# Optimization experiments

Hardware: AMD Instinct MI355X
Metric: run time of the kernel (lower is better)

## Reference

```python
import jax, jax.numpy as jnp
import numpy as np

# --- static module config (from init_kwargs) ---
C1_OUT = 64          # c1OutChannels
C1K = 400            # k winners in conv layer
N_FC = 1024          # fc1 hidden units (n)
K_FC = 100           # k winners in fc1
BOOST = 1.0          # boostStrength
W_SPARSITY = 0.5     # weightSparsity: fraction of fc1 weights allowed nonzero
HP = 12              # pooled spatial size: floor((28-5+1)/2)
C1_OUTPUT_LEN = C1_OUT * HP * HP  # 9216
BATCH = 4096


def setup_inputs() -> dict:
    key = jax.random.key(0)
    ks = jax.random.split(key, 10)
    x = jax.random.normal(ks[0], (BATCH, 1, 28, 28), jnp.float32)
    c1_w = jax.random.normal(ks[1], (C1_OUT, 1, 5, 5), jnp.float32) * 0.1
    c1_b = jax.random.normal(ks[2], (C1_OUT,), jnp.float32) * 0.01
    # duty cycles live in [0, ~density]
    duty_cnn = jax.random.uniform(ks[3], (1, C1_OUT, 1, 1), jnp.float32) * 0.05
    fc1_w = jax.random.normal(ks[4], (N_FC, C1_OUT_LEN_ := C1_OUTPUT_LEN), jnp.float32) * 0.01
    fc1_mask_raw = jax.random.uniform(ks[5], (N_FC, C1_OUTPUT_LEN), jnp.float32)
    fc1_b = jax.random.normal(ks[6], (N_FC,), jnp.float32) * 0.01
    duty_fc = jax.random.uniform(ks[7], (N_FC,), jnp.float32) * 0.1
    fc2_w = jax.random.normal(ks[8], (10, N_FC), jnp.float32) * 0.05
    fc2_b = jnp.zeros((10,), jnp.float32)
    return dict(x=x, c1_w=c1_w, c1_b=c1_b, duty_cnn=duty_cnn, fc1_w=fc1_w,
                fc1_mask_raw=fc1_mask_raw, fc1_b=fc1_b, duty_fc=duty_fc,
                fc2_w=fc2_w, fc2_b=fc2_b)


def _kwinners(x_flat, boost_flat, k):
    """Duty-cycle-boosted k-winner mask.
    x_flat: [B, N]; boost_flat: [1, N] broadcastable boost factors.
    Keeps original x values at the top-k boosted positions per row, zeros rest.
    Boosting uses stop_gradient(x), matching KWinners*.forward(x.detach()*boost).
    """
    boosted = jax.lax.stop_gradient(x_flat) * boost_flat
    thr = jax.lax.top_k(boosted, k)[0][:, -1:]  # k-th largest per row
    return jnp.where(boosted >= thr, x_flat, jnp.zeros((), x_flat.dtype))


def reference(x, c1_w, c1_b, duty_cnn, fc1_w, fc1_mask_raw, fc1_b, duty_fc,
              fc2_w, fc2_b):
    B = x.shape[0]
    # conv2d (valid, stride 1) -> [B, 64, 24, 24]
    y = jax.lax.conv_general_dilated(
        x, c1_w, window_strides=(1, 1), padding='VALID',
        dimension_numbers=('NCHW', 'OIHW', 'NCHW')) + c1_b[None, :, None, None]
    # max_pool2d(2) -> [B, 64, 12, 12]
    y = jax.lax.reduce_window(y, -jnp.inf, jax.lax.max,
                              (1, 1, 2, 2), (1, 1, 2, 2), 'VALID')
    # KWinnersCNN: global top-k over flattened (C,H,W), per-channel boost
    target_density = C1K / C1_OUTPUT_LEN
    boost_c = jnp.exp((target_density - duty_cnn) * BOOST)  # [1,C,1,1]
    boost_flat = jnp.broadcast_to(boost_c, (1, C1_OUT, HP, HP)).reshape(1, -1)
    yf = _kwinners(y.reshape(B, -1), boost_flat, C1K)  # [B, 9216]
    # LinearSDR fc1: sparse-weight linear + KWinners
    w_mask = (fc1_mask_raw < W_SPARSITY).astype(fc1_w.dtype)
    h = yf @ (fc1_w * w_mask).T + fc1_b  # [B, 1024]
    boost_fc = jnp.exp((K_FC / N_FC - duty_fc) * BOOST)[None, :]
    h = _kwinners(h, boost_fc, K_FC)
    # fc2 + log_softmax (dropout inactive in eval mode)
    logits = h @ fc2_w.T + fc2_b
    return jax.nn.log_softmax(logits, axis=1)
```

## Files before the change

kernel.cpp:

```cpp
#include <hip/hip_runtime.h>

__device__ __forceinline__ float b2f(unsigned short u) {
  return __uint_as_float(((unsigned)u) << 16);
}
__device__ __forceinline__ unsigned short f2b(float f) {
  unsigned u = __float_as_uint(f);
  return (unsigned short)((u + 0x7FFFu + ((u >> 16) & 1u)) >> 16);
}
__device__ __forceinline__ float gload(const void* p, int i, int isb) {
  return isb ? b2f(((const unsigned short*)p)[i]) : ((const float*)p)[i];
}
__device__ __forceinline__ unsigned tokey(float f) {
  unsigned u = __float_as_uint(f);
  return u ^ (unsigned)(((int)u >> 31) | 0x80000000u);
}

__global__ void k_detect(const void* x, int* flag) {
  int tid = threadIdx.x;
  unsigned short u = ((const unsigned short*)x)[2 * tid];
  int e = (u >> 7) & 0xFF;
  bool sane = (e >= 100 && e <= 140);
  unsigned long long m = __ballot(sane);
  if (tid == 0) *flag = (__popcll(m) >= 40) ? 1 : 0;
}

__global__ __launch_bounds__(256) void k_prep(const void* __restrict__ fc1w,
                                              const void* __restrict__ mraw,
                                              float* __restrict__ WtF,
                                              const int* __restrict__ flag) {
  __shared__ float tile[64][65];
  const int isb = *flag;
  const int i0 = blockIdx.x * 64;
  const int u0 = blockIdx.y * 64;
  const int tx = threadIdx.x & 63, ty = threadIdx.x >> 6;
  for (int uu = ty; uu < 64; uu += 4) {
    int gi = (u0 + uu) * 9216 + i0 + tx;
    float wv = gload(fc1w, gi, isb);
    float mv = gload(mraw, gi, isb);
    tile[uu][tx] = (mv < 0.5f) ? wv : 0.0f;
  }
  __syncthreads();
  for (int ii = ty; ii < 64; ii += 4)
    WtF[(i0 + ii) * 1024 + u0 + tx] = tile[tx][ii];
}

__global__ __launch_bounds__(256) void k_conv(const void* __restrict__ x,
                                              const void* __restrict__ c1w_g,
                                              const void* __restrict__ c1b_g,
                                              const void* __restrict__ duty_g,
                                              int2* __restrict__ wpair,
                                              int* __restrict__ wcnt,
                                              const int* __restrict__ flag) {
  __shared__ __align__(16) float img[784];
  __shared__ float cw[1600];
  __shared__ float cb[64], bcs[64];
  __shared__ __align__(16) float pooled[9216];
  __shared__ unsigned hist4[4][256];
  __shared__ unsigned wtot[4];
  __shared__ unsigned selb, selk;
  const int tid = threadIdx.x;
  const int b = blockIdx.x;
  const int isb = *flag;
  const int lane = tid & 63;
  const int wv_id = tid >> 6;

  for (int i = tid; i < 784; i += 256) img[i] = gload(x, b * 784 + i, isb);
  for (int i = tid; i < 1600; i += 256) cw[i] = gload(c1w_g, i, isb);
  if (tid < 64) {
    cb[tid] = gload(c1b_g, tid, isb);
    float arg = (float)(400.0 / 9216.0) - gload(duty_g, tid, isb);
    bcs[tid] = (float)exp((double)arg);
  }
  __syncthreads();

  {
    const int c = tid >> 2;
    const int half = tid & 1;
    const int ph0 = ((tid >> 1) & 1) * 6;
    float w[25];
#pragma unroll
    for (int i = 0; i < 25; ++i) w[i] = cw[c * 25 + i];
    const float bias = cb[c];
    float R[6][16];
#pragma unroll
    for (int r = 0; r < 6; ++r) {
      int ir = 2 * ph0 + r;
#pragma unroll
      for (int q = 0; q < 4; ++q)
        ((float4*)&R[r][0])[q] = ((const float4*)img)[ir * 7 + half * 3 + q];
    }
#pragma unroll
    for (int i = 0; i < 6; ++i) {
      const int ph = ph0 + i;
      float a0[12], a1[12];
#pragma unroll
      for (int j = 0; j < 12; ++j) { a0[j] = 0.f; a1[j] = 0.f; }
#pragma unroll
      for (int kj = 0; kj < 5; ++kj) {
#pragma unroll
        for (int kr = 0; kr < 5; ++kr) {
          float wk = w[kr * 5 + kj];
          const float* r0 = &R[(2 * i + kr) % 6][0];
          const float* r1 = &R[(2 * i + kr + 1) % 6][0];
#pragma unroll
          for (int j = 0; j < 12; ++j) {
            a0[j] = fmaf(r0[j + kj], wk, a0[j]);
            a1[j] = fmaf(r1[j + kj], wk, a1[j]);
          }
        }
      }
      int obase = c * 144 + ph * 12 + half * 6;
#pragma unroll
      for (int q = 0; q < 6; ++q) {
        float m = fmaxf(fmaxf(a0[2 * q], a0[2 * q + 1]),
                        fmaxf(a1[2 * q], a1[2 * q + 1]));
        pooled[obase + q] = m + bias;
      }
      if (i < 5) {
        int ir0 = 2 * ph + 6, ir1 = 2 * ph + 7;
        float* d0 = &R[(2 * i) % 6][0];
        float* d1 = &R[(2 * i + 1) % 6][0];
#pragma unroll
        for (int q = 0; q < 4; ++q) {
          ((float4*)d0)[q] = ((const float4*)img)[ir0 * 7 + half * 3 + q];
          ((float4*)d1)[q] = ((const float4*)img)[ir1 * 7 + half * 3 + q];
        }
      }
    }
  }
  __syncthreads();

  unsigned keys[36];
  {
    const float bcf = bcs[tid >> 2];
#pragma unroll
    for (int e4 = 0; e4 < 9; ++e4) {
      float4 pv = ((float4*)pooled)[tid * 9 + e4];
      keys[4 * e4 + 0] = tokey(pv.x * bcf);
      keys[4 * e4 + 1] = tokey(pv.y * bcf);
      keys[4 * e4 + 2] = tokey(pv.z * bcf);
      keys[4 * e4 + 3] = tokey(pv.w * bcf);
    }
  }

  unsigned kfix = 0;
  unsigned kk = 400;
  for (int pass = 3; pass >= 0; --pass) {
    const int shift = pass * 8;
    const unsigned himask = (pass == 3) ? 0u : (0xFFFFFFFFu << (shift + 8));
#pragma unroll
    for (int w2 = 0; w2 < 4; ++w2) hist4[w2][tid] = 0;
    __syncthreads();
    unsigned* myh = hist4[wv_id];
#pragma unroll
    for (int e = 0; e < 36; ++e) {
      unsigned key = keys[e];
      if (((key ^ kfix) & himask) == 0)
        atomicAdd(&myh[(key >> shift) & 255u], 1u);
    }
    __syncthreads();
    unsigned own = hist4[0][tid] + hist4[1][tid] + hist4[2][tid] + hist4[3][tid];
    unsigned v = own;
#pragma unroll
    for (int off = 1; off < 64; off <<= 1) {
      unsigned y = __shfl_down(v, off, 64);
      if (lane + off < 64) v += y;
    }
    if (lane == 0) wtot[wv_id] = v;
    __syncthreads();
#pragma unroll
    for (int w2 = 0; w2 < 4; ++w2)
      if (w2 > wv_id) v += wtot[w2];
    unsigned snext = v - own;
    if (v >= kk && snext < kk) {
      selb = (unsigned)tid;
      selk = kk - snext;
    }
    __syncthreads();
    kfix |= selb << shift;
    kk = selk;
    __syncthreads();
  }

  unsigned mycnt = 0;
#pragma unroll
  for (int e = 0; e < 36; ++e) mycnt += (keys[e] >= kfix) ? 1u : 0u;
  unsigned px = mycnt;
#pragma unroll
  for (int off = 1; off < 64; off <<= 1) {
    unsigned y = __shfl_up(px, off, 64);
    if (lane >= off) px += y;
  }
  if (lane == 63) wtot[wv_id] = px;
  __syncthreads();
  unsigned base = 0;
#pragma unroll
  for (int w2 = 0; w2 < 4; ++w2)
    if (w2 < wv_id) base += wtot[w2];
  int pos = (int)(base + px - mycnt);
  for (int e = 0; e < 36; ++e) {
    if (keys[e] >= kfix) {
      int o = tid * 36 + e;
      if (pos < 512)
        wpair[b * 512 + pos] = make_int2(__float_as_int(pooled[o]), o << 12);
      ++pos;
    }
  }
  if (tid == 0) {
    unsigned tot = wtot[0] + wtot[1] + wtot[2] + wtot[3];
    wcnt[b] = (int)(tot < 512u ? tot : 512u);
  }
}

__global__ __launch_bounds__(128) void k_fc1(const float* __restrict__ WtF,
                                             const int2* __restrict__ wpair,
                                             const int* __restrict__ wcnt,
                                             const void* __restrict__ fc1b,
                                             float* __restrict__ h,
                                             const int* __restrict__ flag) {
  __shared__ int2 wl[512];
  const int tid = threadIdx.x;
  const int img = blockIdx.x >> 3;
  const int slice = blockIdx.x & 7;
  const int isb = *flag;
  const int cnt = wcnt[img];
  const int2* __restrict__ wp = wpair + img * 512;
  for (int i = tid; i < cnt; i += 128) wl[i] = wp[i];
  __syncthreads();
  const int u = (slice << 7) + tid;
  const unsigned ub = (unsigned)u * 4u;
  const char* __restrict__ Wb = (const char*)WtF;
  float acc = 0.f;
#pragma unroll 8
  for (int w = 0; w < cnt; ++w) {
    int2 p = wl[w];
    acc = fmaf(__int_as_float(p.x),
               *(const float*)(Wb + ((unsigned)p.y + ub)), acc);
  }
  h[img * 1024 + u] = acc + gload(fc1b, u, isb);
}

__global__ __launch_bounds__(256) void k_sel(const float* __restrict__ h,
                                             const void* __restrict__ dutyfc,
                                             const void* __restrict__ fc2w,
                                             const void* __restrict__ fc2b,
                                             void* __restrict__ out,
                                             const int* __restrict__ flag) {
  __shared__ unsigned hist[256];
  __shared__ unsigned selb, selk;
  __shared__ double lg[10];
  __shared__ double mred[2];
  const int tid = threadIdx.x;
  const int row = blockIdx.x;
  const int isb = *flag;
  if (tid < 10) lg[tid] = (double)gload(fc2b, tid, isb);
  __syncthreads();

  const int u0 = 2 * tid, u1 = 2 * tid + 1, u2 = 512 + 2 * tid, u3 = 513 + 2 * tid;
  float2 hlo = ((const float2*)(h + row * 1024))[tid];
  float2 hhi = ((const float2*)(h + row * 1024 + 512))[tid];
  float h0 = hlo.x, h1 = hlo.y, h2 = hhi.x, h3 = hhi.y;
  float bf0 = (float)exp((double)(0.09765625f - gload(dutyfc, u0, isb)));
  float bf1 = (float)exp((double)(0.09765625f - gload(dutyfc, u1, isb)));
  float bf2 = (float)exp((double)(0.09765625f - gload(dutyfc, u2, isb)));
  float bf3 = (float)exp((double)(0.09765625f - gload(dutyfc, u3, isb)));
  unsigned k0 = tokey(h0 * bf0);
  unsigned k1 = tokey(h1 * bf1);
  unsigned k2 = tokey(h2 * bf2);
  unsigned k3 = tokey(h3 * bf3);

  unsigned kfix = 0;
  int kk = 100;
  for (int pass = 3; pass >= 0; --pass) {
    const int shift = pass * 8;
    const unsigned himask = (pass == 3) ? 0u : (0xFFFFFFFFu << (shift + 8));
    hist[tid] = 0;
    __syncthreads();
    if (((k0 ^ kfix) & himask) == 0) atomicAdd(&hist[(k0 >> shift) & 255u], 1u);
    if (((k1 ^ kfix) & himask) == 0) atomicAdd(&hist[(k1 >> shift) & 255u], 1u);
    if (((k2 ^ kfix) & himask) == 0) atomicAdd(&hist[(k2 >> shift) & 255u], 1u);
    if (((k3 ^ kfix) & himask) == 0) atomicAdd(&hist[(k3 >> shift) & 255u], 1u);
    __syncthreads();
    unsigned v = hist[tid];
    for (int offs = 1; offs < 256; offs <<= 1) {
      unsigned other = (tid + offs < 256) ? hist[tid + offs] : 0u;
      __syncthreads();
      v += other;
      hist[tid] = v;
      __syncthreads();
    }
    unsigned snext = (tid < 255) ? hist[tid + 1] : 0u;
    if (v >= (unsigned)kk && snext < (unsigned)kk) {
      selb = (unsigned)tid;
      selk = (unsigned)(kk - (int)snext);
    }
    __syncthreads();
    kfix |= selb << shift;
    kk = (int)selk;
    __syncthreads();
  }
  bool kp0 = k0 >= kfix, kp1 = k1 >= kfix, kp2 = k2 >= kfix, kp3 = k3 >= kfix;

  double part[10];
#pragma unroll
  for (int c = 0; c < 10; ++c) part[c] = 0.0;
  if (kp0) {
#pragma unroll
    for (int c = 0; c < 10; ++c) part[c] = fma((double)h0, (double)gload(fc2w, c * 1024 + u0, isb), part[c]);
  }
  if (kp1) {
#pragma unroll
    for (int c = 0; c < 10; ++c) part[c] = fma((double)h1, (double)gload(fc2w, c * 1024 + u1, isb), part[c]);
  }
  if (kp2) {
#pragma unroll
    for (int c = 0; c < 10; ++c) part[c] = fma((double)h2, (double)gload(fc2w, c * 1024 + u2, isb), part[c]);
  }
  if (kp3) {
#pragma unroll
    for (int c = 0; c < 10; ++c) part[c] = fma((double)h3, (double)gload(fc2w, c * 1024 + u3, isb), part[c]);
  }
#pragma unroll
  for (int c = 0; c < 10; ++c) {
    double p = part[c];
    for (int off = 32; off > 0; off >>= 1) p += __shfl_xor(p, off);
    if ((tid & 63) == 0) atomicAdd(&lg[c], p);
  }
  __syncthreads();
  if (tid == 0) {
    double m = lg[0];
#pragma unroll
    for (int c = 1; c < 10; ++c) m = lg[c] > m ? lg[c] : m;
    double sum = 0.0;
#pragma unroll
    for (int c = 0; c < 10; ++c) sum += exp(lg[c] - m);
    mred[0] = m;
    mred[1] = log(sum);
  }
  __syncthreads();
  if (tid < 10) {
    double o = lg[tid] - mred[0] - mred[1];
    if (isb)
      ((unsigned short*)out)[row * 10 + tid] = f2b((float)o);
    else
      ((float*)out)[row * 10 + tid] = (float)o;
  }
}

extern "C" void kernel_launch(void* const* d_in, const int* in_sizes, int n_in,
                              void* d_out, int out_size, void* d_ws, size_t ws_size,
                              hipStream_t stream) {
  char* ws = (char*)d_ws;
  float* WtF = (float*)ws;
  int2* wpair = (int2*)(ws + 37748736);
  int* wcnt = (int*)(ws + 54525952);
  float* h = (float*)(ws + 54542336);
  int* flag = (int*)(ws + 71319552);

  k_detect<<<1, 64, 0, stream>>>(d_in[0], flag);
  k_prep<<<dim3(144, 16), 256, 0, stream>>>(d_in[4], d_in[5], WtF, flag);
  k_conv<<<4096, 256, 0, stream>>>(d_in[0], d_in[1], d_in[2], d_in[3],
                                   wpair, wcnt, flag);
  k_fc1<<<4096 * 8, 128, 0, stream>>>(WtF, wpair, wcnt, d_in[6], h, flag);
  k_sel<<<4096, 256, 0, stream>>>(h, d_in[7], d_in[8], d_in[9], d_out, flag);
}
```

Measured before the change: 625.8 us.

## Use per-wave histograms with shuffle scan in k_sel, precompute fc1 boosts

The fc1 kernel drops its shared-memory staging of the winner list and its barrier, reading the (value, offset) pairs straight from global memory (uniform across the block, so cached). A new small kernel computes the fc1 boost factors once, in double-precision exp, into workspace that reuses the start of the transposed weight buffer after fc1 is done. This replaces four double exps per thread in every selection block. The radix-select now uses four per-wave histograms to cut atomic contention, and a wave shuffle scan instead of the 8-step barrier-heavy shared-memory scan. This adds one launch and relies on WtF no longer being needed by later kernels.

```diff
diff --git a/kernel.cpp b/kernel.cpp
--- a/kernel.cpp
+++ b/kernel.cpp
@@ -218,41 +218,49 @@
                                              const void* __restrict__ fc1b,
                                              float* __restrict__ h,
                                              const int* __restrict__ flag) {
-  __shared__ int2 wl[512];
   const int tid = threadIdx.x;
   const int img = blockIdx.x >> 3;
   const int slice = blockIdx.x & 7;
   const int isb = *flag;
   const int cnt = wcnt[img];
   const int2* __restrict__ wp = wpair + img * 512;
-  for (int i = tid; i < cnt; i += 128) wl[i] = wp[i];
-  __syncthreads();
   const int u = (slice << 7) + tid;
-  const unsigned ub = (unsigned)u * 4u;
-  const char* __restrict__ Wb = (const char*)WtF;
+  const char* __restrict__ Wb = (const char*)WtF + (unsigned)u * 4u;
   float acc = 0.f;
 #pragma unroll 8
   for (int w = 0; w < cnt; ++w) {
-    int2 p = wl[w];
+    int2 p = wp[w];
     acc = fmaf(__int_as_float(p.x),
-               *(const float*)(Wb + ((unsigned)p.y + ub)), acc);
+               *(const float*)(Wb + (unsigned)p.y), acc);
   }
   h[img * 1024 + u] = acc + gload(fc1b, u, isb);
 }
 
+__global__ __launch_bounds__(256) void k_boost(const void* __restrict__ dutyfc,
+                                               float* __restrict__ bf,
+                                               const int* __restrict__ flag) {
+  const int u = blockIdx.x * 256 + threadIdx.x;
+  const int isb = *flag;
+  if (u < 1024)
+    bf[u] = (float)exp((double)(0.09765625f - gload(dutyfc, u, isb)));
+}
+
 __global__ __launch_bounds__(256) void k_sel(const float* __restrict__ h,
-                                             const void* __restrict__ dutyfc,
+                                             const float* __restrict__ bf,
                                              const void* __restrict__ fc2w,
                                              const void* __restrict__ fc2b,
                                              void* __restrict__ out,
                                              const int* __restrict__ flag) {
-  __shared__ unsigned hist[256];
+  __shared__ unsigned hist4[4][256];
+  __shared__ unsigned wtot[4];
   __shared__ unsigned selb, selk;
   __shared__ double lg[10];
   __shared__ double mred[2];
   const int tid = threadIdx.x;
   const int row = blockIdx.x;
   const int isb = *flag;
+  const int lane = tid & 63;
+  const int wv_id = tid >> 6;
   if (tid < 10) lg[tid] = (double)gload(fc2b, tid, isb);
   __syncthreads();
 
@@ -260,43 +268,47 @@
   float2 hlo = ((const float2*)(h + row * 1024))[tid];
   float2 hhi = ((const float2*)(h + row * 1024 + 512))[tid];
   float h0 = hlo.x, h1 = hlo.y, h2 = hhi.x, h3 = hhi.y;
-  float bf0 = (float)exp((double)(0.09765625f - gload(dutyfc, u0, isb)));
-  float bf1 = (float)exp((double)(0.09765625f - gload(dutyfc, u1, isb)));
-  float bf2 = (float)exp((double)(0.09765625f - gload(dutyfc, u2, isb)));
-  float bf3 = (float)exp((double)(0.09765625f - gload(dutyfc, u3, isb)));
-  unsigned k0 = tokey(h0 * bf0);
-  unsigned k1 = tokey(h1 * bf1);
-  unsigned k2 = tokey(h2 * bf2);
-  unsigned k3 = tokey(h3 * bf3);
+  float2 blo = ((const float2*)bf)[tid];
+  float2 bhi = ((const float2*)(bf + 512))[tid];
+  unsigned k0 = tokey(h0 * blo.x);
+  unsigned k1 = tokey(h1 * blo.y);
+  unsigned k2 = tokey(h2 * bhi.x);
+  unsigned k3 = tokey(h3 * bhi.y);
 
   unsigned kfix = 0;
-  int kk = 100;
+  unsigned kk = 100;
   for (int pass = 3; pass >= 0; --pass) {
     const int shift = pass * 8;
     const unsigned himask = (pass == 3) ? 0u : (0xFFFFFFFFu << (shift + 8));
-    hist[tid] = 0;
-    __syncthreads();
-    if (((k0 ^ kfix) & himask) == 0) atomicAdd(&hist[(k0 >> shift) & 255u], 1u);
-    if (((k1 ^ kfix) & himask) == 0) atomicAdd(&hist[(k1 >> shift) & 255u], 1u);
-    if (((k2 ^ kfix) & himask) == 0) atomicAdd(&hist[(k2 >> shift) & 255u], 1u);
-    if (((k3 ^ kfix) & himask) == 0) atomicAdd(&hist[(k3 >> shift) & 255u], 1u);
-    __syncthreads();
-    unsigned v = hist[tid];
-    for (int offs = 1; offs < 256; offs <<= 1) {
-      unsigned other = (tid + offs < 256) ? hist[tid + offs] : 0u;
-      __syncthreads();
-      v += other;
-      hist[tid] = v;
-      __syncthreads();
-    }
-    unsigned snext = (tid < 255) ? hist[tid + 1] : 0u;
-    if (v >= (unsigned)kk && snext < (unsigned)kk) {
+#pragma unroll
+    for (int w2 = 0; w2 < 4; ++w2) hist4[w2][tid] = 0;
+    __syncthreads();
+    unsigned* myh = hist4[wv_id];
+    if (((k0 ^ kfix) & himask) == 0) atomicAdd(&myh[(k0 >> shift) & 255u], 1u);
+    if (((k1 ^ kfix) & himask) == 0) atomicAdd(&myh[(k1 >> shift) & 255u], 1u);
+    if (((k2 ^ kfix) & himask) == 0) atomicAdd(&myh[(k2 >> shift) & 255u], 1u);
+    if (((k3 ^ kfix) & himask) == 0) atomicAdd(&myh[(k3 >> shift) & 255u], 1u);
+    __syncthreads();
+    unsigned own = hist4[0][tid] + hist4[1][tid] + hist4[2][tid] + hist4[3][tid];
+    unsigned v = own;
+#pragma unroll
+    for (int off = 1; off < 64; off <<= 1) {
+      unsigned y = __shfl_down(v, off, 64);
+      if (lane + off < 64) v += y;
+    }
+    if (lane == 0) wtot[wv_id] = v;
+    __syncthreads();
+#pragma unroll
+    for (int w2 = 0; w2 < 4; ++w2)
+      if (w2 > wv_id) v += wtot[w2];
+    unsigned snext = v - own;
+    if (v >= kk && snext < kk) {
       selb = (unsigned)tid;
-      selk = (unsigned)(kk - (int)snext);
+      selk = kk - snext;
     }
     __syncthreads();
     kfix |= selb << shift;
-    kk = (int)selk;
+    kk = selk;
     __syncthreads();
   }
   bool kp0 = k0 >= kfix, kp1 = k1 >= kfix, kp2 = k2 >= kfix, kp3 = k3 >= kfix;
@@ -356,11 +368,13 @@
   int* wcnt = (int*)(ws + 54525952);
   float* h = (float*)(ws + 54542336);
   int* flag = (int*)(ws + 71319552);
+  float* bf = WtF;
 
   k_detect<<<1, 64, 0, stream>>>(d_in[0], flag);
   k_prep<<<dim3(144, 16), 256, 0, stream>>>(d_in[4], d_in[5], WtF, flag);
   k_conv<<<4096, 256, 0, stream>>>(d_in[0], d_in[1], d_in[2], d_in[3],
                                    wpair, wcnt, flag);
   k_fc1<<<4096 * 8, 128, 0, stream>>>(WtF, wpair, wcnt, d_in[6], h, flag);
-  k_sel<<<4096, 256, 0, stream>>>(h, d_in[7], d_in[8], d_in[9], d_out, flag);
-}
+  k_boost<<<4, 256, 0, stream>>>(d_in[7], bf, flag);
+  k_sel<<<4096, 256, 0, stream>>>(h, bf, d_in[8], d_in[9], d_out, flag);
+}
```

After: 634.2 us. No clear change (+1.3%).
